# Kernel tuning notes

Measured on AMD Instinct MI355X. Metric: run time of the kernel, lower is better.

The kernel has to match this reference:

```python
import jax, jax.numpy as jnp
import numpy as np

B, S, F_IN, E = 8, 1024, 256, 512
INNER = 2 * E            # mLSTM proj_factor = 2.0
NH = 4                   # mLSTM num_heads
DH = INNER // NH
KS = 4                   # causal conv1d kernel size
QKV_BS = 4               # qkv_proj_blocksize
NB = INNER // QKV_BS     # number of block-diagonal qkv blocks


def setup_inputs() -> dict:
    key = jax.random.key(0)
    ks = jax.random.split(key, 16)
    g = lambda k, shape, scale: jax.random.normal(k, shape, jnp.float32) * scale
    return {
        "x": g(ks[0], (B, S, F_IN), 1.0),
        "W_in": g(ks[1], (E, F_IN), F_IN ** -0.5),
        "b_in": jnp.zeros((E,), jnp.float32),
        "ln1_w": jnp.ones((E,), jnp.float32),
        "W_up": g(ks[2], (2 * INNER, E), E ** -0.5),
        "conv_w": g(ks[3], (INNER, 1, KS), KS ** -0.5),
        "conv_b": jnp.zeros((INNER,), jnp.float32),
        "Wq": g(ks[4], (NB, QKV_BS, QKV_BS), QKV_BS ** -0.5),
        "Wk": g(ks[5], (NB, QKV_BS, QKV_BS), QKV_BS ** -0.5),
        "Wv": g(ks[6], (NB, QKV_BS, QKV_BS), QKV_BS ** -0.5),
        "W_ig": g(ks[7], (NH, 3 * INNER), (3 * INNER) ** -0.5),
        "b_ig": jnp.zeros((NH,), jnp.float32),
        "W_fg": g(ks[8], (NH, 3 * INNER), (3 * INNER) ** -0.5),
        "b_fg": jnp.linspace(3.0, 6.0, NH, dtype=jnp.float32),  # xlstm fgate bias init
        "mhln_w": jnp.ones((INNER,), jnp.float32),
        "skip": jnp.ones((INNER,), jnp.float32),
        "W_down": g(ks[9], (E, INNER), INNER ** -0.5),
        "ln_post_w": jnp.ones((E,), jnp.float32),
    }


def _ln(h, w, eps=1e-5):
    m = h.mean(-1, keepdims=True)
    v = jnp.mean((h - m) ** 2, axis=-1, keepdims=True)
    return (h - m) * jax.lax.rsqrt(v + eps) * w


def _causal_conv(x, w, b):
    # x: (B,S,C) -> depthwise causal conv, kernel KS, left-pad KS-1
    y = jax.lax.conv_general_dilated(
        x.transpose(0, 2, 1), w, (1,), [(KS - 1, 0)],
        dimension_numbers=("NCH", "OIH", "NCH"), feature_group_count=INNER)
    return y.transpose(0, 2, 1) + b


def _headwise(x, W):
    # block-diagonal linear (LinearHeadwiseExpand, bias=False)
    b, s, _ = x.shape
    xh = x.reshape(b, s, NB, QKV_BS)
    return jnp.einsum("bsni,noi->bsno", xh, W).reshape(b, s, -1)


def reference(x, W_in, b_in, ln1_w, W_up, conv_w, conv_b, Wq, Wk, Wv,
              W_ig, b_ig, W_fg, b_fg, mhln_w, skip, W_down, ln_post_w):
    # input proj (+ dropout = identity in eval)
    xp = x @ W_in.T + b_in                                  # (B,S,E)
    res = xp
    h = _ln(xp, ln1_w)                                      # pre-LN of mLSTM block
    up = h @ W_up.T                                         # (B,S,2*INNER)
    x_m, z = up[..., :INNER], up[..., INNER:]
    xc = jax.nn.silu(_causal_conv(x_m, conv_w, conv_b))     # (B,S,INNER)
    q = _headwise(xc, Wq)
    k = _headwise(xc, Wk)
    v = _headwise(x_m, Wv)
    gate_in = jnp.concatenate([q, k, v], axis=-1)           # (B,S,3*INNER)
    ig = (gate_in @ W_ig.T + b_ig).transpose(0, 2, 1)       # (B,NH,S)
    fg = (gate_in @ W_fg.T + b_fg).transpose(0, 2, 1)       # (B,NH,S)
    to_h = lambda t: t.reshape(B, S, NH, DH).transpose(0, 2, 1, 3)
    qh, kh, vh = to_h(q), to_h(k), to_h(v)                  # (B,NH,S,DH)
    # --- parallel_stabilized_simple mLSTM backend ---
    logf = jax.nn.log_sigmoid(fg)                           # (B,NH,S)
    a = jnp.concatenate([jnp.zeros_like(logf[..., :1]), jnp.cumsum(logf, -1)], -1)
    M = a[..., :, None] - a[..., None, :]                   # (B,NH,S+1,S+1)
    mask = jnp.tril(jnp.ones((S + 1, S + 1), bool))
    logD = jnp.where(mask, M, -jnp.inf)[..., 1:, 1:] + ig[..., None, :]
    maxD = logD.max(-1, keepdims=True)                      # (B,NH,S,1)
    D = jnp.exp(logD - maxD)
    C = jnp.einsum("bnsd,bntd->bnst", qh, kh * (DH ** -0.5)) * D
    n = jnp.maximum(jnp.abs(C.sum(-1, keepdims=True)), jnp.exp(-maxD))
    hh = jnp.einsum("bnst,bntd->bnsd", C / (n + 1e-6), vh)  # (B,NH,S,DH)
    # multi-head layernorm (GroupNorm per head, weight only, bias-free)
    hn = hh.transpose(0, 2, 1, 3)                           # (B,S,NH,DH)
    mu = hn.mean(-1, keepdims=True)
    var = jnp.mean((hn - mu) ** 2, axis=-1, keepdims=True)
    hn = (hn - mu) * jax.lax.rsqrt(var + 1e-5) * mhln_w.reshape(NH, DH)
    hn = hn.reshape(B, S, INNER)
    h_state = (hn + skip * xc) * jax.nn.silu(z)             # learnable skip + output gate
    y = h_state @ W_down.T                                  # (B,S,E)
    out = res + y                                           # residual
    return _ln(out, ln_post_w)                              # post_blocks_norm
```

## Files before the change

kernel.cpp:

```cpp
#include <hip/hip_runtime.h>

#define S_LEN 1024
#define B_SZ 8
#define F_IN_D 256
#define E_DIM 512
#define INNER_D 1024
#define NH_D 4
#define DH_D 256
#define NROW (B_SZ * S_LEN)

typedef _Float16 half8 __attribute__((ext_vector_type(8)));
typedef _Float16 half4_t __attribute__((ext_vector_type(4)));
typedef float v4f __attribute__((ext_vector_type(4)));

__global__ __launch_bounds__(256) void cast4_kernel(
    const float* __restrict__ s0, const float* __restrict__ s1,
    const float* __restrict__ s2, const float* __restrict__ s3,
    _Float16* __restrict__ d0, _Float16* __restrict__ d1,
    _Float16* __restrict__ d2, _Float16* __restrict__ d3,
    int n0, int n1, int n2, int n3)
{
  int i = (blockIdx.x * 256 + threadIdx.x) * 4;
  const float* s; _Float16* d; int off;
  if (i < n0)                { s = s0; d = d0; off = i; }
  else if (i < n0 + n1)      { s = s1; d = d1; off = i - n0; }
  else if (i < n0 + n1 + n2) { s = s2; d = d2; off = i - n0 - n1; }
  else if (i < n0 + n1 + n2 + n3) { s = s3; d = d3; off = i - n0 - n1 - n2; }
  else return;
  float4 v = *(const float4*)(s + off);
  half4_t o = {(_Float16)v.x, (_Float16)v.y, (_Float16)v.z, (_Float16)v.w};
  *(half4_t*)(d + off) = o;
}

#define GBM 128
#define GBN 128
#define GBK 64
#define LDKG (GBK + 8)

__global__ __launch_bounds__(256) void gemm_h16(
    const _Float16* __restrict__ A, const _Float16* __restrict__ B,
    const float* __restrict__ bias, float* __restrict__ C,
    int M, int N, int K)
{
  __shared__ __align__(16) _Float16 As[GBM][LDKG];
  __shared__ __align__(16) _Float16 Bs[GBN][LDKG];
  const int tid = threadIdx.x;
  const int lane = tid & 63, w = tid >> 6;
  const int wr = w >> 1, wc = w & 1;
  const int quad = lane >> 4, l16 = lane & 15;
  const int bm = blockIdx.y * GBM, bn = blockIdx.x * GBN;
  const int srow = tid >> 1;
  const int scol = (tid & 1) * 32;

  v4f acc[4][4];
#pragma unroll
  for (int i = 0; i < 4; ++i)
#pragma unroll
    for (int j = 0; j < 4; ++j) acc[i][j] = (v4f){0.f, 0.f, 0.f, 0.f};

  const _Float16* Ap = A + (size_t)(bm + srow) * K + scol;
  const _Float16* Bp = B + (size_t)(bn + srow) * K + scol;
  half8 ap[4], bp[4];
#pragma unroll
  for (int j = 0; j < 4; ++j) {
    ap[j] = *(const half8*)(Ap + j * 8);
    bp[j] = *(const half8*)(Bp + j * 8);
  }

  for (int k0 = 0; k0 < K; k0 += GBK) {
    __syncthreads();
#pragma unroll
    for (int j = 0; j < 4; ++j) {
      *(half8*)(&As[srow][scol + j * 8]) = ap[j];
      *(half8*)(&Bs[srow][scol + j * 8]) = bp[j];
    }
    __syncthreads();
    if (k0 + GBK < K) {
      const int kn = k0 + GBK;
#pragma unroll
      for (int j = 0; j < 4; ++j) {
        ap[j] = *(const half8*)(Ap + kn + j * 8);
        bp[j] = *(const half8*)(Bp + kn + j * 8);
      }
    }
#pragma unroll
    for (int kc = 0; kc < 2; ++kc) {
      half8 af[4], bf[4];
#pragma unroll
      for (int i = 0; i < 4; ++i)
        af[i] = *(const half8*)(&As[wr * 64 + i * 16 + l16][kc * 32 + quad * 8]);
#pragma unroll
      for (int j = 0; j < 4; ++j)
        bf[j] = *(const half8*)(&Bs[wc * 64 + j * 16 + l16][kc * 32 + quad * 8]);
#pragma unroll
      for (int i = 0; i < 4; ++i)
#pragma unroll
        for (int j = 0; j < 4; ++j)
          acc[i][j] = __builtin_amdgcn_mfma_f32_16x16x32_f16(af[i], bf[j], acc[i][j], 0, 0, 0);
    }
  }

#pragma unroll
  for (int j = 0; j < 4; ++j) {
    const int col = bn + wc * 64 + j * 16 + l16;
    const float bv = bias ? bias[col] : 0.f;
#pragma unroll
    for (int i = 0; i < 4; ++i) {
      const int row0 = bm + wr * 64 + i * 16 + quad * 4;
#pragma unroll
      for (int r = 0; r < 4; ++r)
        C[(size_t)(row0 + r) * N + col] = acc[i][j][r] + bv;
    }
  }
}

__global__ __launch_bounds__(256) void gemm_h16_up(
    const _Float16* __restrict__ A, const _Float16* __restrict__ B,
    _Float16* __restrict__ xmh, _Float16* __restrict__ szb,
    int M, int N, int K)
{
  __shared__ __align__(16) _Float16 As[GBM][LDKG];
  __shared__ __align__(16) _Float16 Bs[GBN][LDKG];
  const int tid = threadIdx.x;
  const int lane = tid & 63, w = tid >> 6;
  const int wr = w >> 1, wc = w & 1;
  const int quad = lane >> 4, l16 = lane & 15;
  const int bm = blockIdx.y * GBM, bn = blockIdx.x * GBN;
  const int srow = tid >> 1;
  const int scol = (tid & 1) * 32;

  v4f acc[4][4];
#pragma unroll
  for (int i = 0; i < 4; ++i)
#pragma unroll
    for (int j = 0; j < 4; ++j) acc[i][j] = (v4f){0.f, 0.f, 0.f, 0.f};

  const _Float16* Ap = A + (size_t)(bm + srow) * K + scol;
  const _Float16* Bp = B + (size_t)(bn + srow) * K + scol;
  half8 ap[4], bp[4];
#pragma unroll
  for (int j = 0; j < 4; ++j) {
    ap[j] = *(const half8*)(Ap + j * 8);
    bp[j] = *(const half8*)(Bp + j * 8);
  }

  for (int k0 = 0; k0 < K; k0 += GBK) {
    __syncthreads();
#pragma unroll
    for (int j = 0; j < 4; ++j) {
      *(half8*)(&As[srow][scol + j * 8]) = ap[j];
      *(half8*)(&Bs[srow][scol + j * 8]) = bp[j];
    }
    __syncthreads();
    if (k0 + GBK < K) {
      const int kn = k0 + GBK;
#pragma unroll
      for (int j = 0; j < 4; ++j) {
        ap[j] = *(const half8*)(Ap + kn + j * 8);
        bp[j] = *(const half8*)(Bp + kn + j * 8);
      }
    }
#pragma unroll
    for (int kc = 0; kc < 2; ++kc) {
      half8 af[4], bf[4];
#pragma unroll
      for (int i = 0; i < 4; ++i)
        af[i] = *(const half8*)(&As[wr * 64 + i * 16 + l16][kc * 32 + quad * 8]);
#pragma unroll
      for (int j = 0; j < 4; ++j)
        bf[j] = *(const half8*)(&Bs[wc * 64 + j * 16 + l16][kc * 32 + quad * 8]);
#pragma unroll
      for (int i = 0; i < 4; ++i)
#pragma unroll
        for (int j = 0; j < 4; ++j)
          acc[i][j] = __builtin_amdgcn_mfma_f32_16x16x32_f16(af[i], bf[j], acc[i][j], 0, 0, 0);
    }
  }

  const bool zhalf = (bn >= INNER_D);
#pragma unroll
  for (int j = 0; j < 4; ++j) {
    const int col = bn + wc * 64 + j * 16 + l16;
    const int colm = col & (INNER_D - 1);
#pragma unroll
    for (int i = 0; i < 4; ++i) {
      const int row0 = bm + wr * 64 + i * 16 + quad * 4;
#pragma unroll
      for (int r = 0; r < 4; ++r) {
        float a = acc[i][j][r];
        if (zhalf) {
          float s = a / (1.f + __expf(-a));
          szb[(size_t)(row0 + r) * INNER_D + colm] = (_Float16)s;
        } else {
          xmh[(size_t)(row0 + r) * INNER_D + colm] = (_Float16)a;
        }
      }
    }
  }
}

__device__ __forceinline__ float block_sum4(float v, float* red, int tid) {
#pragma unroll
  for (int off = 32; off; off >>= 1) v += __shfl_xor(v, off);
  if ((tid & 63) == 0) red[tid >> 6] = v;
  __syncthreads();
  float t = red[0] + red[1] + red[2] + red[3];
  __syncthreads();
  return t;
}

__global__ __launch_bounds__(256) void ln_mul_kernel(
    const float* __restrict__ in, const float* __restrict__ w,
    _Float16* __restrict__ out)
{
  __shared__ float red[4];
  const int row = blockIdx.x;
  const int tid = threadIdx.x;
  const float* p = in + (size_t)row * E_DIM;
  float v0 = p[tid], v1 = p[tid + 256];
  float mean = block_sum4(v0 + v1, red, tid) * (1.f / E_DIM);
  float d0 = v0 - mean, d1 = v1 - mean;
  float var = block_sum4(d0 * d0 + d1 * d1, red, tid) * (1.f / E_DIM);
  float rstd = rsqrtf(var + 1e-5f);
  out[(size_t)row * E_DIM + tid] = (_Float16)(d0 * rstd * w[tid]);
  out[(size_t)row * E_DIM + tid + 256] = (_Float16)(d1 * rstd * w[tid + 256]);
}

__global__ __launch_bounds__(256) void final_ln_kernel(
    const float* __restrict__ res, const float* __restrict__ y,
    const float* __restrict__ w, float* __restrict__ out)
{
  __shared__ float red[4];
  const int row = blockIdx.x;
  const int tid = threadIdx.x;
  const size_t base = (size_t)row * E_DIM;
  float v0 = res[base + tid] + y[base + tid];
  float v1 = res[base + tid + 256] + y[base + tid + 256];
  float mean = block_sum4(v0 + v1, red, tid) * (1.f / E_DIM);
  float d0 = v0 - mean, d1 = v1 - mean;
  float var = block_sum4(d0 * d0 + d1 * d1, red, tid) * (1.f / E_DIM);
  float rstd = rsqrtf(var + 1e-5f);
  out[base + tid] = d0 * rstd * w[tid];
  out[base + tid + 256] = d1 * rstd * w[tid + 256];
}

__global__ __launch_bounds__(256) void chg_kernel(
    const _Float16* __restrict__ xm, const float* __restrict__ cw,
    const float* __restrict__ cb,
    const float* __restrict__ Wq, const float* __restrict__ Wk,
    const float* __restrict__ Wv,
    const float* __restrict__ Wig, const float* __restrict__ big,
    const float* __restrict__ Wfg, const float* __restrict__ bfg,
    _Float16* __restrict__ xch, _Float16* __restrict__ qh,
    _Float16* __restrict__ khb, _Float16* __restrict__ vhb,
    float* __restrict__ ig, float* __restrict__ fg)
{
  __shared__ float red[4][32];
  const int tid = threadIdx.x;
  const int lane = tid & 63, wid = tid >> 6;
  const int row0 = blockIdx.x * 4;
  const int sl0 = row0 & (S_LEN - 1);
  const int c = tid * 4;

  float t[7][4];
#pragma unroll
  for (int j = 0; j < 7; ++j) {
    const int off = j - 3;
    if (sl0 + off < 0) {
      t[j][0] = t[j][1] = t[j][2] = t[j][3] = 0.f;
    } else {
      half4_t hv = *(const half4_t*)(xm + (size_t)(row0 + off) * INNER_D + c);
      t[j][0] = (float)hv.x; t[j][1] = (float)hv.y;
      t[j][2] = (float)hv.z; t[j][3] = (float)hv.w;
    }
  }
  float wct[4][4];
#pragma unroll
  for (int j = 0; j < 4; ++j) {
    float4 wc4 = *(const float4*)(cw + (c + j) * 4);
    wct[j][0] = wc4.x; wct[j][1] = wc4.y; wct[j][2] = wc4.z; wct[j][3] = wc4.w;
  }
  float4 cb4 = *(const float4*)(cb + c);
  const float cbs[4] = {cb4.x, cb4.y, cb4.z, cb4.w};
  float wqm[16], wkm[16], wvm[16];
#pragma unroll
  for (int i = 0; i < 4; ++i) {
    float4 a = *(const float4*)(Wq + tid * 16 + i * 4);
    float4 bq = *(const float4*)(Wk + tid * 16 + i * 4);
    float4 cq = *(const float4*)(Wv + tid * 16 + i * 4);
    wqm[i * 4] = a.x; wqm[i * 4 + 1] = a.y; wqm[i * 4 + 2] = a.z; wqm[i * 4 + 3] = a.w;
    wkm[i * 4] = bq.x; wkm[i * 4 + 1] = bq.y; wkm[i * 4 + 2] = bq.z; wkm[i * 4 + 3] = bq.w;
    wvm[i * 4] = cq.x; wvm[i * 4 + 1] = cq.y; wvm[i * 4 + 2] = cq.z; wvm[i * 4 + 3] = cq.w;
  }

  float q4[4][4], k4[4][4], v4m[4][4];
#pragma unroll
  for (int r = 0; r < 4; ++r) {
    float xc4[4];
#pragma unroll
    for (int j = 0; j < 4; ++j) {
      float a = cbs[j] + wct[j][0] * t[r][j] + wct[j][1] * t[r + 1][j]
                       + wct[j][2] * t[r + 2][j] + wct[j][3] * t[r + 3][j];
      xc4[j] = a / (1.f + __expf(-a));
    }
#pragma unroll
    for (int i = 0; i < 4; ++i) {
      q4[r][i] = wqm[i * 4] * xc4[0] + wqm[i * 4 + 1] * xc4[1]
               + wqm[i * 4 + 2] * xc4[2] + wqm[i * 4 + 3] * xc4[3];
      k4[r][i] = wkm[i * 4] * xc4[0] + wkm[i * 4 + 1] * xc4[1]
               + wkm[i * 4 + 2] * xc4[2] + wkm[i * 4 + 3] * xc4[3];
      v4m[r][i] = wvm[i * 4] * t[r + 3][0] + wvm[i * 4 + 1] * t[r + 3][1]
                + wvm[i * 4 + 2] * t[r + 3][2] + wvm[i * 4 + 3] * t[r + 3][3];
    }
    const size_t base = (size_t)(row0 + r) * INNER_D + c;
    half4_t xo = {(_Float16)xc4[0], (_Float16)xc4[1], (_Float16)xc4[2], (_Float16)xc4[3]};
    half4_t qo = {(_Float16)q4[r][0], (_Float16)q4[r][1], (_Float16)q4[r][2], (_Float16)q4[r][3]};
    half4_t ko = {(_Float16)k4[r][0], (_Float16)k4[r][1], (_Float16)k4[r][2], (_Float16)k4[r][3]};
    half4_t vo = {(_Float16)v4m[r][0], (_Float16)v4m[r][1], (_Float16)v4m[r][2], (_Float16)v4m[r][3]};
    *(half4_t*)(xch + base) = xo;
    *(half4_t*)(qh + base) = qo;
    *(half4_t*)(khb + base) = ko;
    *(half4_t*)(vhb + base) = vo;
  }

  float vals[32];
#pragma unroll
  for (int g = 0; g < 8; ++g) {
    const float* wb = (g < 4 ? Wig : Wfg) + (g & 3) * 3072 + c;
    float4 w1 = *(const float4*)(wb);
    float4 w2 = *(const float4*)(wb + 1024);
    float4 w3 = *(const float4*)(wb + 2048);
#pragma unroll
    for (int r = 0; r < 4; ++r) {
      vals[g * 4 + r] =
          q4[r][0] * w1.x + q4[r][1] * w1.y + q4[r][2] * w1.z + q4[r][3] * w1.w
        + k4[r][0] * w2.x + k4[r][1] * w2.y + k4[r][2] * w2.z + k4[r][3] * w2.w
        + v4m[r][0] * w3.x + v4m[r][1] * w3.y + v4m[r][2] * w3.z + v4m[r][3] * w3.w;
    }
  }
#pragma unroll
  for (int i = 0; i < 32; ++i) {
    float x = vals[i];
#pragma unroll
    for (int off = 32; off; off >>= 1) x += __shfl_xor(x, off);
    vals[i] = x;
  }
  if (lane == 0) {
#pragma unroll
    for (int i = 0; i < 32; ++i) red[wid][i] = vals[i];
  }
  __syncthreads();
  if (tid < 32) {
    float sm = red[0][tid] + red[1][tid] + red[2][tid] + red[3][tid];
    const int g = tid >> 2, r = tid & 3;
    const int h = g & 3;
    const int b = row0 >> 10;
    const size_t oidx = (size_t)(b * NH_D + h) * S_LEN + sl0 + r;
    if (g < 4) ig[oidx] = sm + big[h];
    else       fg[oidx] = sm + bfg[h];
  }
}

__device__ __forceinline__ float logsigf(float x) {
  return fminf(x, 0.f) - log1pf(__expf(-fabsf(x)));
}

__global__ __launch_bounds__(256) void scan_kernel(
    const float* __restrict__ ig, const float* __restrict__ fg,
    float* __restrict__ m_, float* __restrict__ rmax_, float* __restrict__ maxd_,
    float* __restrict__ em_)
{
  __shared__ float sc[256];
  const int bh = blockIdx.x;
  const int tid = threadIdx.x;
  const size_t base = (size_t)bh * S_LEN + tid * 4;
  float4 f4 = *(const float4*)(fg + base);
  float4 i4 = *(const float4*)(ig + base);
  float l0 = logsigf(f4.x), l1 = logsigf(f4.y), l2 = logsigf(f4.z), l3 = logsigf(f4.w);
  float p0 = l0, p1 = p0 + l1, p2 = p1 + l2, p3 = p2 + l3;
  sc[tid] = p3;
  __syncthreads();
  for (int off = 1; off < 256; off <<= 1) {
    float o = (tid >= off) ? sc[tid - off] : 0.f;
    __syncthreads();
    sc[tid] += o;
    __syncthreads();
  }
  float aoff = (tid == 0) ? 0.f : sc[tid - 1];
  __syncthreads();
  float a0 = aoff + p0, a1 = aoff + p1, a2 = aoff + p2, a3 = aoff + p3;
  float m0 = i4.x - a0, m1 = i4.y - a1, m2 = i4.z - a2, m3 = i4.w - a3;
  float x0 = m0, x1 = fmaxf(x0, m1), x2 = fmaxf(x1, m2), x3 = fmaxf(x2, m3);
  sc[tid] = x3;
  __syncthreads();
  for (int off = 1; off < 256; off <<= 1) {
    float o = (tid >= off) ? sc[tid - off] : -1e30f;
    __syncthreads();
    sc[tid] = fmaxf(sc[tid], o);
    __syncthreads();
  }
  float moff = (tid == 0) ? -1e30f : sc[tid - 1];
  float tmax = sc[tid | 15];
  float r0 = fmaxf(moff, x0), r1 = fmaxf(moff, x1), r2 = fmaxf(moff, x2), r3 = fmaxf(moff, x3);
  const float scale = 0.0625f;
  float4 mo = {m0, m1, m2, m3};
  float4 ro = {r0, r1, r2, r3};
  float4 dd = {a0 + r0, a1 + r1, a2 + r2, a3 + r3};
  float4 eo = {scale * __expf(m0 - tmax), scale * __expf(m1 - tmax),
               scale * __expf(m2 - tmax), scale * __expf(m3 - tmax)};
  *(float4*)(m_ + base) = mo;
  *(float4*)(rmax_ + base) = ro;
  *(float4*)(maxd_ + base) = dd;
  *(float4*)(em_ + base) = eo;
}

__global__ __launch_bounds__(256) void vtrans_kernel(
    const _Float16* __restrict__ vb, _Float16* __restrict__ vt)
{
  __shared__ _Float16 tile[64][68];
  const int b = blockIdx.z, dt = blockIdx.x, st = blockIdx.y;
  const int c4 = (threadIdx.x & 15) * 4, rr = threadIdx.x >> 4;
  const int s0 = st * 64, d0 = dt * 64;
#pragma unroll
  for (int i = 0; i < 4; ++i) {
    int r = rr + i * 16;
    half4_t v = *(const half4_t*)(vb + ((size_t)(b * S_LEN + s0 + r)) * INNER_D + d0 + c4);
    tile[r][c4 + 0] = v.x; tile[r][c4 + 1] = v.y;
    tile[r][c4 + 2] = v.z; tile[r][c4 + 3] = v.w;
  }
  __syncthreads();
#pragma unroll
  for (int i = 0; i < 4; ++i) {
    int dd = rr + i * 16;
    half4_t o = {tile[c4 + 0][dd], tile[c4 + 1][dd], tile[c4 + 2][dd], tile[c4 + 3][dd]};
    *(half4_t*)(vt + ((size_t)(b * INNER_D + d0 + dd)) * S_LEN + s0 + c4) = o;
  }
}

#define KP 264
#define VP 72

__global__ __launch_bounds__(256, 2) void attn_blk_kernel(
    const _Float16* __restrict__ qh, const _Float16* __restrict__ khb,
    const _Float16* __restrict__ vt,
    const float* __restrict__ m_, const float* __restrict__ em,
    const float* __restrict__ rmax_, const float* __restrict__ maxd_,
    const float* __restrict__ mhln_w, const float* __restrict__ skip,
    const _Float16* __restrict__ xch, const _Float16* __restrict__ szb,
    _Float16* __restrict__ hstate)
{
  __shared__ __align__(16) _Float16 Ks[64][KP];
  __shared__ __align__(16) _Float16 Vs[256][VP];
  __shared__ _Float16 plds[4][16][72];
  const int tid = threadIdx.x;
  const int lane = tid & 63, wid = tid >> 6;
  const int quad = lane >> 4, l16 = lane & 15;
  const int bh = blockIdx.x & 31;
  const int pp = blockIdx.x >> 5;
  const int sblk = 15 - pp;
  const int h = bh & 3, b = bh >> 2;
  _Float16 (*P)[72] = plds[wid];
  const float* rmaxp = rmax_ + (size_t)bh * S_LEN;
  const float* emp = em + (size_t)bh * S_LEN;
  const float* mp = m_ + (size_t)bh * S_LEN;
  const float* maxdp = maxd_ + (size_t)bh * S_LEN;
  const float scale = 0.0625f;

  const _Float16* kg = khb + ((size_t)(b * S_LEN)) * INNER_D + h * DH_D;
  const _Float16* vg = vt + ((size_t)(b * INNER_D + h * DH_D)) * S_LEN;
  const int krow_s = tid >> 5;
  const int kcol_s = (tid & 31) * 8;
  const int vrow_s = tid >> 3;
  const int vcol_s = (tid & 7) * 8;

  const int ntile = sblk + 1;
  const int s0 = sblk * 64 + wid * 16;

  half8 kpre[8], vpre[8];
#pragma unroll
  for (int i = 0; i < 8; ++i) {
    kpre[i] = *(const half8*)(kg + (size_t)(i * 8 + krow_s) * INNER_D + kcol_s);
    vpre[i] = *(const half8*)(vg + (size_t)(i * 32 + vrow_s) * S_LEN + vcol_s);
  }

  half8 qf[8];
  const _Float16* qrow = qh + ((size_t)(b * S_LEN + s0 + l16)) * INNER_D + h * DH_D + quad * 8;
#pragma unroll
  for (int c = 0; c < 8; ++c) qf[c] = *(const half8*)(qrow + c * 32);

  v4f acc[16];
#pragma unroll
  for (int nc = 0; nc < 16; ++nc) acc[nc] = (v4f){0.f, 0.f, 0.f, 0.f};
  float rsum[4] = {0.f, 0.f, 0.f, 0.f};
  float rmax_row[4];
#pragma unroll
  for (int r = 0; r < 4; ++r) rmax_row[r] = rmaxp[s0 + quad * 4 + r];

  for (int tt = 0; tt < ntile; ++tt) {
    const int t0 = tt * 64;
    const bool last = (tt + 1 == ntile);
    __syncthreads();
#pragma unroll
    for (int i = 0; i < 8; ++i) {
      *(half8*)(&Ks[i * 8 + krow_s][kcol_s]) = kpre[i];
      *(half8*)(&Vs[i * 32 + vrow_s][vcol_s]) = vpre[i];
    }
    __syncthreads();
    if (!last) {
      const int tn = t0 + 64;
#pragma unroll
      for (int i = 0; i < 8; ++i) {
        kpre[i] = *(const half8*)(kg + (size_t)(tn + i * 8 + krow_s) * INNER_D + kcol_s);
        vpre[i] = *(const half8*)(vg + (size_t)(i * 32 + vrow_s) * S_LEN + tn + vcol_s);
      }
    }
    const bool diag = last;
    float rowfac[4];
    if (!diag) {
      const float rtile = rmaxp[t0 + 63];
#pragma unroll
      for (int r = 0; r < 4; ++r) rowfac[r] = __expf(rtile - rmax_row[r]);
    }
#pragma unroll
    for (int sub = 0; sub < 4; ++sub) {
      v4f sacc0 = (v4f){0.f, 0.f, 0.f, 0.f};
      v4f sacc1 = (v4f){0.f, 0.f, 0.f, 0.f};
#pragma unroll
      for (int c = 0; c < 4; ++c) {
        half8 kf0 = *(const half8*)(&Ks[sub * 16 + l16][c * 32 + quad * 8]);
        half8 kf1 = *(const half8*)(&Ks[sub * 16 + l16][(c + 4) * 32 + quad * 8]);
        sacc0 = __builtin_amdgcn_mfma_f32_16x16x32_f16(qf[c], kf0, sacc0, 0, 0, 0);
        sacc1 = __builtin_amdgcn_mfma_f32_16x16x32_f16(qf[c + 4], kf1, sacc1, 0, 0, 0);
      }
      v4f sacc = sacc0 + sacc1;
      const int t = t0 + sub * 16 + l16;
      if (diag) {
        const float mt = mp[t];
#pragma unroll
        for (int r = 0; r < 4; ++r) {
          const int srow = s0 + quad * 4 + r;
          float cc = (t <= srow) ? sacc[r] * scale * __expf(mt - rmax_row[r]) : 0.f;
          rsum[r] += cc;
          P[quad * 4 + r][sub * 16 + l16] = (_Float16)cc;
        }
      } else {
        const float emv = emp[t];
#pragma unroll
        for (int r = 0; r < 4; ++r) {
          float cc = sacc[r] * emv * rowfac[r];
          rsum[r] += cc;
          P[quad * 4 + r][sub * 16 + l16] = (_Float16)cc;
        }
      }
    }
    asm volatile("s_waitcnt lgkmcnt(0)" ::: "memory");
    half8 pf0 = *(const half8*)(&P[l16][quad * 8]);
    half8 pf1 = *(const half8*)(&P[l16][32 + quad * 8]);
#pragma unroll
    for (int nc = 0; nc < 16; ++nc) {
      half8 vf0 = *(const half8*)(&Vs[nc * 16 + l16][quad * 8]);
      half8 vf1 = *(const half8*)(&Vs[nc * 16 + l16][32 + quad * 8]);
      acc[nc] = __builtin_amdgcn_mfma_f32_16x16x32_f16(pf0, vf0, acc[nc], 0, 0, 0);
      acc[nc] = __builtin_amdgcn_mfma_f32_16x16x32_f16(pf1, vf1, acc[nc], 0, 0, 0);
    }
  }

  float inv[4];
#pragma unroll
  for (int r = 0; r < 4; ++r) {
    float rs = rsum[r];
    rs += __shfl_xor(rs, 1); rs += __shfl_xor(rs, 2);
    rs += __shfl_xor(rs, 4); rs += __shfl_xor(rs, 8);
    float md = maxdp[s0 + quad * 4 + r];
    float n = fmaxf(fabsf(rs), __expf(-md));
    inv[r] = 1.f / (n + 1e-6f);
  }
#pragma unroll
  for (int nc = 0; nc < 16; ++nc) {
#pragma unroll
    for (int r = 0; r < 4; ++r) acc[nc][r] *= inv[r];
  }
  float mean[4], rstd[4];
#pragma unroll
  for (int r = 0; r < 4; ++r) {
    float sm = 0.f;
#pragma unroll
    for (int nc = 0; nc < 16; ++nc) sm += acc[nc][r];
    sm += __shfl_xor(sm, 1); sm += __shfl_xor(sm, 2);
    sm += __shfl_xor(sm, 4); sm += __shfl_xor(sm, 8);
    mean[r] = sm * (1.f / DH_D);
  }
#pragma unroll
  for (int r = 0; r < 4; ++r) {
    float sq = 0.f;
#pragma unroll
    for (int nc = 0; nc < 16; ++nc) { float d = acc[nc][r] - mean[r]; sq += d * d; }
    sq += __shfl_xor(sq, 1); sq += __shfl_xor(sq, 2);
    sq += __shfl_xor(sq, 4); sq += __shfl_xor(sq, 8);
    rstd[r] = rsqrtf(sq * (1.f / DH_D) + 1e-5f);
  }
#pragma unroll
  for (int nc = 0; nc < 16; ++nc) {
    const int d = h * DH_D + nc * 16 + l16;
    const float w = mhln_w[d];
    const float sk = skip[d];
#pragma unroll
    for (int r = 0; r < 4; ++r) {
      const size_t row = (size_t)(b * S_LEN + s0 + quad * 4 + r);
      float xcv = (float)xch[row * INNER_D + d];
      float sz = (float)szb[row * INNER_D + d];
      float o = ((acc[nc][r] - mean[r]) * rstd[r] * w + sk * xcv) * sz;
      hstate[row * INNER_D + d] = (_Float16)o;
    }
  }
}

extern "C" void kernel_launch(void* const* d_in, const int* in_sizes, int n_in,
                              void* d_out, int out_size, void* d_ws, size_t ws_size,
                              hipStream_t stream)
{
  const float* x      = (const float*)d_in[0];
  const float* W_in   = (const float*)d_in[1];
  const float* b_in   = (const float*)d_in[2];
  const float* ln1_w  = (const float*)d_in[3];
  const float* W_up   = (const float*)d_in[4];
  const float* conv_w = (const float*)d_in[5];
  const float* conv_b = (const float*)d_in[6];
  const float* Wq     = (const float*)d_in[7];
  const float* Wk     = (const float*)d_in[8];
  const float* Wv     = (const float*)d_in[9];
  const float* W_ig   = (const float*)d_in[10];
  const float* b_ig   = (const float*)d_in[11];
  const float* W_fg   = (const float*)d_in[12];
  const float* b_fg   = (const float*)d_in[13];
  const float* mhln_w = (const float*)d_in[14];
  const float* skip   = (const float*)d_in[15];
  const float* W_down = (const float*)d_in[16];
  const float* ln_post_w = (const float*)d_in[17];
  float* out = (float*)d_out;

  float* ws = (float*)d_ws;
  size_t o = 0;
  float* xp     = ws + o; o += (size_t)NROW * E_DIM;
  float* hbuf   = ws + o; o += (size_t)NROW * E_DIM;
  _Float16* h16 = (_Float16*)(ws + o);
  size_t ho = 0;
  _Float16* xh      = h16 + ho; ho += (size_t)NROW * F_IN_D;
  _Float16* WinH    = h16 + ho; ho += (size_t)E_DIM * F_IN_D;
  _Float16* WupH    = h16 + ho; ho += (size_t)2 * INNER_D * E_DIM;
  _Float16* WdownH  = h16 + ho; ho += (size_t)E_DIM * INNER_D;
  _Float16* hh      = h16 + ho; ho += (size_t)NROW * E_DIM;
  _Float16* xmh     = h16 + ho; ho += (size_t)NROW * INNER_D;
  _Float16* szb     = h16 + ho; ho += (size_t)NROW * INNER_D;
  _Float16* xch     = h16 + ho; ho += (size_t)NROW * INNER_D;
  _Float16* qh      = h16 + ho; ho += (size_t)NROW * INNER_D;
  _Float16* khb     = h16 + ho; ho += (size_t)NROW * INNER_D;
  _Float16* vhb     = h16 + ho; ho += (size_t)NROW * INNER_D;
  _Float16* vtb     = h16 + ho; ho += (size_t)NROW * INNER_D;
  _Float16* hstateH = h16 + ho; ho += (size_t)NROW * INNER_D;

  const int GSZ = B_SZ * NH_D * S_LEN;
  float* igb   = hbuf;
  float* fgb   = hbuf + GSZ;
  float* mb    = hbuf + 2 * GSZ;
  float* rmaxb = hbuf + 3 * GSZ;
  float* maxdb = hbuf + 4 * GSZ;
  float* emb   = hbuf + 5 * GSZ;
  float* yb    = hbuf;

  dim3 blk(256);
  const int nx = NROW * F_IN_D, nwi = E_DIM * F_IN_D,
            nwu = 2 * INNER_D * E_DIM, nwd = E_DIM * INNER_D;
  const int ntot = nx + nwi + nwu + nwd;
  cast4_kernel<<<(ntot / 4 + 255) / 256, blk, 0, stream>>>(
      x, W_in, W_up, W_down, xh, WinH, WupH, WdownH, nx, nwi, nwu, nwd);
  gemm_h16<<<dim3(E_DIM / GBN, NROW / GBM), blk, 0, stream>>>(
      xh, WinH, b_in, xp, NROW, E_DIM, F_IN_D);
  ln_mul_kernel<<<NROW, blk, 0, stream>>>(xp, ln1_w, hh);
  gemm_h16_up<<<dim3(2 * INNER_D / GBN, NROW / GBM), blk, 0, stream>>>(
      hh, WupH, xmh, szb, NROW, 2 * INNER_D, E_DIM);
  chg_kernel<<<NROW / 4, blk, 0, stream>>>(
      xmh, conv_w, conv_b, Wq, Wk, Wv, W_ig, b_ig, W_fg, b_fg,
      xch, qh, khb, vhb, igb, fgb);
  scan_kernel<<<B_SZ * NH_D, blk, 0, stream>>>(igb, fgb, mb, rmaxb, maxdb, emb);
  vtrans_kernel<<<dim3(16, 16, 8), blk, 0, stream>>>(vhb, vtb);
  attn_blk_kernel<<<512, blk, 0, stream>>>(
      qh, khb, vtb, mb, emb, rmaxb, maxdb, mhln_w, skip, xch, szb, hstateH);
  gemm_h16<<<dim3(E_DIM / GBN, NROW / GBM), blk, 0, stream>>>(
      hstateH, WdownH, nullptr, yb, NROW, E_DIM, INNER_D);
  final_ln_kernel<<<NROW, blk, 0, stream>>>(xp, yb, ln_post_w, out);
}
```

Measured before the change: 281.6 us.

## Retile mLSTM attention waves into 2x2 grid sharing K/V fragments

```diff
diff --git a/kernel.cpp b/kernel.cpp
--- a/kernel.cpp
+++ b/kernel.cpp
@@ -439,6 +439,7 @@
 
 #define KP 264
 #define VP 72
+#define PP 72
 
 __global__ __launch_bounds__(256, 2) void attn_blk_kernel(
     const _Float16* __restrict__ qh, const _Float16* __restrict__ khb,
@@ -451,15 +452,18 @@
 {
   __shared__ __align__(16) _Float16 Ks[64][KP];
   __shared__ __align__(16) _Float16 Vs[256][VP];
-  __shared__ _Float16 plds[4][16][72];
+  __shared__ __align__(16) _Float16 Pl[64][PP];
+  __shared__ float cred[2][64];
   const int tid = threadIdx.x;
   const int lane = tid & 63, wid = tid >> 6;
   const int quad = lane >> 4, l16 = lane & 15;
+  const int wr = wid >> 1;
+  const int ws = wid & 1;
   const int bh = blockIdx.x & 31;
-  const int pp = blockIdx.x >> 5;
+  int pp = blockIdx.x >> 5;
+  if (pp >= 8) pp = 23 - pp;
   const int sblk = 15 - pp;
   const int h = bh & 3, b = bh >> 2;
-  _Float16 (*P)[72] = plds[wid];
   const float* rmaxp = rmax_ + (size_t)bh * S_LEN;
   const float* emp = em + (size_t)bh * S_LEN;
   const float* mp = m_ + (size_t)bh * S_LEN;
@@ -474,7 +478,7 @@
   const int vcol_s = (tid & 7) * 8;
 
   const int ntile = sblk + 1;
-  const int s0 = sblk * 64 + wid * 16;
+  const int qb0 = sblk * 64;
 
   half8 kpre[8], vpre[8];
 #pragma unroll
@@ -483,18 +487,28 @@
     vpre[i] = *(const half8*)(vg + (size_t)(i * 32 + vrow_s) * S_LEN + vcol_s);
   }
 
-  half8 qf[8];
-  const _Float16* qrow = qh + ((size_t)(b * S_LEN + s0 + l16)) * INNER_D + h * DH_D + quad * 8;
-#pragma unroll
-  for (int c = 0; c < 8; ++c) qf[c] = *(const half8*)(qrow + c * 32);
-
-  v4f acc[16];
-#pragma unroll
-  for (int nc = 0; nc < 16; ++nc) acc[nc] = (v4f){0.f, 0.f, 0.f, 0.f};
-  float rsum[4] = {0.f, 0.f, 0.f, 0.f};
-  float rmax_row[4];
-#pragma unroll
-  for (int r = 0; r < 4; ++r) rmax_row[r] = rmaxp[s0 + quad * 4 + r];
+  half8 qf[2][8];
+#pragma unroll
+  for (int g = 0; g < 2; ++g) {
+    const _Float16* qrow =
+        qh + ((size_t)(b * S_LEN + qb0 + wr * 32 + g * 16 + l16)) * INNER_D
+           + h * DH_D + quad * 8;
+#pragma unroll
+    for (int c = 0; c < 8; ++c) qf[g][c] = *(const half8*)(qrow + c * 32);
+  }
+
+  v4f acc[2][8];
+#pragma unroll
+  for (int g = 0; g < 2; ++g)
+#pragma unroll
+    for (int nc = 0; nc < 8; ++nc) acc[g][nc] = (v4f){0.f, 0.f, 0.f, 0.f};
+  float rsum[8] = {0.f, 0.f, 0.f, 0.f, 0.f, 0.f, 0.f, 0.f};
+  float rmax_row[8];
+#pragma unroll
+  for (int g = 0; g < 2; ++g)
+#pragma unroll
+    for (int r = 0; r < 4; ++r)
+      rmax_row[g * 4 + r] = rmaxp[qb0 + wr * 32 + g * 16 + quad * 4 + r];
 
   for (int tt = 0; tt < ntile; ++tt) {
     const int t0 = tt * 64;
@@ -514,104 +528,153 @@
         vpre[i] = *(const half8*)(vg + (size_t)(i * 32 + vrow_s) * S_LEN + tn + vcol_s);
       }
     }
-    const bool diag = last;
-    float rowfac[4];
-    if (!diag) {
+    float rowfac[8];
+    if (!last) {
       const float rtile = rmaxp[t0 + 63];
 #pragma unroll
-      for (int r = 0; r < 4; ++r) rowfac[r] = __expf(rtile - rmax_row[r]);
-    }
-#pragma unroll
-    for (int sub = 0; sub < 4; ++sub) {
-      v4f sacc0 = (v4f){0.f, 0.f, 0.f, 0.f};
-      v4f sacc1 = (v4f){0.f, 0.f, 0.f, 0.f};
-#pragma unroll
-      for (int c = 0; c < 4; ++c) {
-        half8 kf0 = *(const half8*)(&Ks[sub * 16 + l16][c * 32 + quad * 8]);
-        half8 kf1 = *(const half8*)(&Ks[sub * 16 + l16][(c + 4) * 32 + quad * 8]);
-        sacc0 = __builtin_amdgcn_mfma_f32_16x16x32_f16(qf[c], kf0, sacc0, 0, 0, 0);
-        sacc1 = __builtin_amdgcn_mfma_f32_16x16x32_f16(qf[c + 4], kf1, sacc1, 0, 0, 0);
+      for (int gr = 0; gr < 8; ++gr) rowfac[gr] = __expf(rtile - rmax_row[gr]);
+    }
+#pragma unroll
+    for (int ks = 0; ks < 2; ++ks) {
+      v4f sg[2];
+      sg[0] = (v4f){0.f, 0.f, 0.f, 0.f};
+      sg[1] = (v4f){0.f, 0.f, 0.f, 0.f};
+#pragma unroll
+      for (int c = 0; c < 8; ++c) {
+        half8 kf = *(const half8*)(&Ks[ws * 32 + ks * 16 + l16][c * 32 + quad * 8]);
+        sg[0] = __builtin_amdgcn_mfma_f32_16x16x32_f16(qf[0][c], kf, sg[0], 0, 0, 0);
+        sg[1] = __builtin_amdgcn_mfma_f32_16x16x32_f16(qf[1][c], kf, sg[1], 0, 0, 0);
       }
-      v4f sacc = sacc0 + sacc1;
-      const int t = t0 + sub * 16 + l16;
-      if (diag) {
+      const int t = t0 + ws * 32 + ks * 16 + l16;
+      if (last) {
         const float mt = mp[t];
 #pragma unroll
-        for (int r = 0; r < 4; ++r) {
-          const int srow = s0 + quad * 4 + r;
-          float cc = (t <= srow) ? sacc[r] * scale * __expf(mt - rmax_row[r]) : 0.f;
-          rsum[r] += cc;
-          P[quad * 4 + r][sub * 16 + l16] = (_Float16)cc;
-        }
+        for (int g = 0; g < 2; ++g)
+#pragma unroll
+          for (int r = 0; r < 4; ++r) {
+            const int srow = qb0 + wr * 32 + g * 16 + quad * 4 + r;
+            float cc = (t <= srow)
+                         ? sg[g][r] * scale * __expf(mt - rmax_row[g * 4 + r]) : 0.f;
+            rsum[g * 4 + r] += cc;
+            Pl[wr * 32 + g * 16 + quad * 4 + r][ws * 32 + ks * 16 + l16] = (_Float16)cc;
+          }
       } else {
         const float emv = emp[t];
 #pragma unroll
-        for (int r = 0; r < 4; ++r) {
-          float cc = sacc[r] * emv * rowfac[r];
-          rsum[r] += cc;
-          P[quad * 4 + r][sub * 16 + l16] = (_Float16)cc;
-        }
+        for (int g = 0; g < 2; ++g)
+#pragma unroll
+          for (int r = 0; r < 4; ++r) {
+            float cc = sg[g][r] * emv * rowfac[g * 4 + r];
+            rsum[g * 4 + r] += cc;
+            Pl[wr * 32 + g * 16 + quad * 4 + r][ws * 32 + ks * 16 + l16] = (_Float16)cc;
+          }
       }
     }
-    asm volatile("s_waitcnt lgkmcnt(0)" ::: "memory");
-    half8 pf0 = *(const half8*)(&P[l16][quad * 8]);
-    half8 pf1 = *(const half8*)(&P[l16][32 + quad * 8]);
-#pragma unroll
-    for (int nc = 0; nc < 16; ++nc) {
-      half8 vf0 = *(const half8*)(&Vs[nc * 16 + l16][quad * 8]);
-      half8 vf1 = *(const half8*)(&Vs[nc * 16 + l16][32 + quad * 8]);
-      acc[nc] = __builtin_amdgcn_mfma_f32_16x16x32_f16(pf0, vf0, acc[nc], 0, 0, 0);
-      acc[nc] = __builtin_amdgcn_mfma_f32_16x16x32_f16(pf1, vf1, acc[nc], 0, 0, 0);
-    }
-  }
-
-  float inv[4];
-#pragma unroll
-  for (int r = 0; r < 4; ++r) {
-    float rs = rsum[r];
+    __syncthreads();
+    half8 pf[2][2];
+#pragma unroll
+    for (int g = 0; g < 2; ++g) {
+      pf[g][0] = *(const half8*)(&Pl[wr * 32 + g * 16 + l16][quad * 8]);
+      pf[g][1] = *(const half8*)(&Pl[wr * 32 + g * 16 + l16][32 + quad * 8]);
+    }
+#pragma unroll
+    for (int nc = 0; nc < 8; ++nc) {
+      half8 vf0 = *(const half8*)(&Vs[ws * 128 + nc * 16 + l16][quad * 8]);
+      half8 vf1 = *(const half8*)(&Vs[ws * 128 + nc * 16 + l16][32 + quad * 8]);
+      acc[0][nc] = __builtin_amdgcn_mfma_f32_16x16x32_f16(pf[0][0], vf0, acc[0][nc], 0, 0, 0);
+      acc[0][nc] = __builtin_amdgcn_mfma_f32_16x16x32_f16(pf[0][1], vf1, acc[0][nc], 0, 0, 0);
+      acc[1][nc] = __builtin_amdgcn_mfma_f32_16x16x32_f16(pf[1][0], vf0, acc[1][nc], 0, 0, 0);
+      acc[1][nc] = __builtin_amdgcn_mfma_f32_16x16x32_f16(pf[1][1], vf1, acc[1][nc], 0, 0, 0);
+    }
+  }
+
+#pragma unroll
+  for (int gr = 0; gr < 8; ++gr) {
+    float rs = rsum[gr];
     rs += __shfl_xor(rs, 1); rs += __shfl_xor(rs, 2);
     rs += __shfl_xor(rs, 4); rs += __shfl_xor(rs, 8);
-    float md = maxdp[s0 + quad * 4 + r];
-    float n = fmaxf(fabsf(rs), __expf(-md));
-    inv[r] = 1.f / (n + 1e-6f);
-  }
-#pragma unroll
-  for (int nc = 0; nc < 16; ++nc) {
-#pragma unroll
-    for (int r = 0; r < 4; ++r) acc[nc][r] *= inv[r];
-  }
-  float mean[4], rstd[4];
-#pragma unroll
-  for (int r = 0; r < 4; ++r) {
+    rsum[gr] = rs;
+  }
+  if (l16 == 0) {
+#pragma unroll
+    for (int g = 0; g < 2; ++g)
+#pragma unroll
+      for (int r = 0; r < 4; ++r)
+        cred[ws][wr * 32 + g * 16 + quad * 4 + r] = rsum[g * 4 + r];
+  }
+  __syncthreads();
+  float inv[8];
+#pragma unroll
+  for (int g = 0; g < 2; ++g)
+#pragma unroll
+    for (int r = 0; r < 4; ++r) {
+      const int row = wr * 32 + g * 16 + quad * 4 + r;
+      float rs = cred[0][row] + cred[1][row];
+      float md = maxdp[qb0 + row];
+      float n = fmaxf(fabsf(rs), __expf(-md));
+      inv[g * 4 + r] = 1.f / (n + 1e-6f);
+    }
+#pragma unroll
+  for (int g = 0; g < 2; ++g)
+#pragma unroll
+    for (int nc = 0; nc < 8; ++nc)
+#pragma unroll
+      for (int r = 0; r < 4; ++r) acc[g][nc][r] *= inv[g * 4 + r];
+
+  __syncthreads();
+  float mean[8];
+#pragma unroll
+  for (int gr = 0; gr < 8; ++gr) {
+    const int g = gr >> 2, r = gr & 3;
     float sm = 0.f;
 #pragma unroll
-    for (int nc = 0; nc < 16; ++nc) sm += acc[nc][r];
+    for (int nc = 0; nc < 8; ++nc) sm += acc[g][nc][r];
     sm += __shfl_xor(sm, 1); sm += __shfl_xor(sm, 2);
     sm += __shfl_xor(sm, 4); sm += __shfl_xor(sm, 8);
-    mean[r] = sm * (1.f / DH_D);
-  }
-#pragma unroll
-  for (int r = 0; r < 4; ++r) {
+    if (l16 == 0) cred[ws][wr * 32 + g * 16 + quad * 4 + r] = sm;
+  }
+  __syncthreads();
+#pragma unroll
+  for (int gr = 0; gr < 8; ++gr) {
+    const int g = gr >> 2, r = gr & 3;
+    const int row = wr * 32 + g * 16 + quad * 4 + r;
+    mean[gr] = (cred[0][row] + cred[1][row]) * (1.f / DH_D);
+  }
+  __syncthreads();
+  float rstd[8];
+#pragma unroll
+  for (int gr = 0; gr < 8; ++gr) {
+    const int g = gr >> 2, r = gr & 3;
     float sq = 0.f;
 #pragma unroll
-    for (int nc = 0; nc < 16; ++nc) { float d = acc[nc][r] - mean[r]; sq += d * d; }
+    for (int nc = 0; nc < 8; ++nc) { float d = acc[g][nc][r] - mean[gr]; sq += d * d; }
     sq += __shfl_xor(sq, 1); sq += __shfl_xor(sq, 2);
     sq += __shfl_xor(sq, 4); sq += __shfl_xor(sq, 8);
-    rstd[r] = rsqrtf(sq * (1.f / DH_D) + 1e-5f);
-  }
-#pragma unroll
-  for (int nc = 0; nc < 16; ++nc) {
-    const int d = h * DH_D + nc * 16 + l16;
+    if (l16 == 0) cred[ws][wr * 32 + g * 16 + quad * 4 + r] = sq;
+  }
+  __syncthreads();
+#pragma unroll
+  for (int gr = 0; gr < 8; ++gr) {
+    const int g = gr >> 2, r = gr & 3;
+    const int row = wr * 32 + g * 16 + quad * 4 + r;
+    rstd[gr] = rsqrtf((cred[0][row] + cred[1][row]) * (1.f / DH_D) + 1e-5f);
+  }
+
+#pragma unroll
+  for (int nc = 0; nc < 8; ++nc) {
+    const int d = h * DH_D + ws * 128 + nc * 16 + l16;
     const float w = mhln_w[d];
     const float sk = skip[d];
 #pragma unroll
-    for (int r = 0; r < 4; ++r) {
-      const size_t row = (size_t)(b * S_LEN + s0 + quad * 4 + r);
-      float xcv = (float)xch[row * INNER_D + d];
-      float sz = (float)szb[row * INNER_D + d];
-      float o = ((acc[nc][r] - mean[r]) * rstd[r] * w + sk * xcv) * sz;
-      hstate[row * INNER_D + d] = (_Float16)o;
-    }
+    for (int g = 0; g < 2; ++g)
+#pragma unroll
+      for (int r = 0; r < 4; ++r) {
+        const size_t row = (size_t)(b * S_LEN + qb0 + wr * 32 + g * 16 + quad * 4 + r);
+        float xcv = (float)xch[row * INNER_D + d];
+        float sz = (float)szb[row * INNER_D + d];
+        float o = ((acc[g][nc][r] - mean[g * 4 + r]) * rstd[g * 4 + r] * w + sk * xcv) * sz;
+        hstate[row * INNER_D + d] = (_Float16)o;
+      }
   }
 }
 
```

Result: no change. 283.9 us (+0.8%).

## Use direct global-to-LDS loads with double-buffered swizzled tiles in fp16 GEMMs

Applied to the files above, without the earlier changes.

```diff
diff --git a/kernel.cpp b/kernel.cpp
--- a/kernel.cpp
+++ b/kernel.cpp
@@ -32,25 +32,35 @@
   *(half4_t*)(d + off) = o;
 }
 
+__device__ __forceinline__ void gl_lds16(const _Float16* g, _Float16* l) {
+  __builtin_amdgcn_global_load_lds(
+      (const __attribute__((address_space(1))) void*)g,
+      (__attribute__((address_space(3))) void*)l, 16, 0, 0);
+}
+
 #define GBM 128
 #define GBN 128
 #define GBK 64
-#define LDKG (GBK + 8)
 
 __global__ __launch_bounds__(256) void gemm_h16(
     const _Float16* __restrict__ A, const _Float16* __restrict__ B,
     const float* __restrict__ bias, float* __restrict__ C,
     int M, int N, int K)
 {
-  __shared__ __align__(16) _Float16 As[GBM][LDKG];
-  __shared__ __align__(16) _Float16 Bs[GBN][LDKG];
+  __shared__ __align__(16) _Float16 As[2][GBM][GBK];
+  __shared__ __align__(16) _Float16 Bs[2][GBN][GBK];
   const int tid = threadIdx.x;
   const int lane = tid & 63, w = tid >> 6;
   const int wr = w >> 1, wc = w & 1;
   const int quad = lane >> 4, l16 = lane & 15;
   const int bm = blockIdx.y * GBM, bn = blockIdx.x * GBN;
-  const int srow = tid >> 1;
-  const int scol = (tid & 1) * 32;
+
+  const int srow = lane >> 3;
+  const int scolh = ((lane & 7) * 8) ^ (srow << 3);
+  const _Float16* Ag = A + (size_t)(bm + w * 32 + srow) * K + scolh;
+  const _Float16* Bg = B + (size_t)(bn + w * 32 + srow) * K + scolh;
+
+  const int rswz = (l16 & 7) << 3;
 
   v4f acc[4][4];
 #pragma unroll
@@ -58,29 +68,21 @@
 #pragma unroll
     for (int j = 0; j < 4; ++j) acc[i][j] = (v4f){0.f, 0.f, 0.f, 0.f};
 
-  const _Float16* Ap = A + (size_t)(bm + srow) * K + scol;
-  const _Float16* Bp = B + (size_t)(bn + srow) * K + scol;
-  half8 ap[4], bp[4];
-#pragma unroll
-  for (int j = 0; j < 4; ++j) {
-    ap[j] = *(const half8*)(Ap + j * 8);
-    bp[j] = *(const half8*)(Bp + j * 8);
-  }
-
+#pragma unroll
+  for (int i = 0; i < 4; ++i) {
+    gl_lds16(Ag + (size_t)(i * 8) * K, &As[0][w * 32 + i * 8][0]);
+    gl_lds16(Bg + (size_t)(i * 8) * K, &Bs[0][w * 32 + i * 8][0]);
+  }
+  __syncthreads();
+
+  int buf = 0;
   for (int k0 = 0; k0 < K; k0 += GBK) {
-    __syncthreads();
-#pragma unroll
-    for (int j = 0; j < 4; ++j) {
-      *(half8*)(&As[srow][scol + j * 8]) = ap[j];
-      *(half8*)(&Bs[srow][scol + j * 8]) = bp[j];
-    }
-    __syncthreads();
     if (k0 + GBK < K) {
       const int kn = k0 + GBK;
 #pragma unroll
-      for (int j = 0; j < 4; ++j) {
-        ap[j] = *(const half8*)(Ap + kn + j * 8);
-        bp[j] = *(const half8*)(Bp + kn + j * 8);
+      for (int i = 0; i < 4; ++i) {
+        gl_lds16(Ag + (size_t)(i * 8) * K + kn, &As[buf ^ 1][w * 32 + i * 8][0]);
+        gl_lds16(Bg + (size_t)(i * 8) * K + kn, &Bs[buf ^ 1][w * 32 + i * 8][0]);
       }
     }
 #pragma unroll
@@ -88,16 +90,18 @@
       half8 af[4], bf[4];
 #pragma unroll
       for (int i = 0; i < 4; ++i)
-        af[i] = *(const half8*)(&As[wr * 64 + i * 16 + l16][kc * 32 + quad * 8]);
+        af[i] = *(const half8*)(&As[buf][wr * 64 + i * 16 + l16][(kc * 32 + quad * 8) ^ rswz]);
 #pragma unroll
       for (int j = 0; j < 4; ++j)
-        bf[j] = *(const half8*)(&Bs[wc * 64 + j * 16 + l16][kc * 32 + quad * 8]);
+        bf[j] = *(const half8*)(&Bs[buf][wc * 64 + j * 16 + l16][(kc * 32 + quad * 8) ^ rswz]);
 #pragma unroll
       for (int i = 0; i < 4; ++i)
 #pragma unroll
         for (int j = 0; j < 4; ++j)
           acc[i][j] = __builtin_amdgcn_mfma_f32_16x16x32_f16(af[i], bf[j], acc[i][j], 0, 0, 0);
     }
+    __syncthreads();
+    buf ^= 1;
   }
 
 #pragma unroll
@@ -119,15 +123,19 @@
     _Float16* __restrict__ xmh, _Float16* __restrict__ szb,
     int M, int N, int K)
 {
-  __shared__ __align__(16) _Float16 As[GBM][LDKG];
-  __shared__ __align__(16) _Float16 Bs[GBN][LDKG];
+  __shared__ __align__(16) _Float16 As[2][GBM][GBK];
+  __shared__ __align__(16) _Float16 Bs[2][GBN][GBK];
   const int tid = threadIdx.x;
   const int lane = tid & 63, w = tid >> 6;
   const int wr = w >> 1, wc = w & 1;
   const int quad = lane >> 4, l16 = lane & 15;
   const int bm = blockIdx.y * GBM, bn = blockIdx.x * GBN;
-  const int srow = tid >> 1;
-  const int scol = (tid & 1) * 32;
+
+  const int srow = lane >> 3;
+  const int scolh = ((lane & 7) * 8) ^ (srow << 3);
+  const _Float16* Ag = A + (size_t)(bm + w * 32 + srow) * K + scolh;
+  const _Float16* Bg = B + (size_t)(bn + w * 32 + srow) * K + scolh;
+  const int rswz = (l16 & 7) << 3;
 
   v4f acc[4][4];
 #pragma unroll
@@ -135,29 +143,21 @@
 #pragma unroll
     for (int j = 0; j < 4; ++j) acc[i][j] = (v4f){0.f, 0.f, 0.f, 0.f};
 
-  const _Float16* Ap = A + (size_t)(bm + srow) * K + scol;
-  const _Float16* Bp = B + (size_t)(bn + srow) * K + scol;
-  half8 ap[4], bp[4];
-#pragma unroll
-  for (int j = 0; j < 4; ++j) {
-    ap[j] = *(const half8*)(Ap + j * 8);
-    bp[j] = *(const half8*)(Bp + j * 8);
-  }
-
+#pragma unroll
+  for (int i = 0; i < 4; ++i) {
+    gl_lds16(Ag + (size_t)(i * 8) * K, &As[0][w * 32 + i * 8][0]);
+    gl_lds16(Bg + (size_t)(i * 8) * K, &Bs[0][w * 32 + i * 8][0]);
+  }
+  __syncthreads();
+
+  int buf = 0;
   for (int k0 = 0; k0 < K; k0 += GBK) {
-    __syncthreads();
-#pragma unroll
-    for (int j = 0; j < 4; ++j) {
-      *(half8*)(&As[srow][scol + j * 8]) = ap[j];
-      *(half8*)(&Bs[srow][scol + j * 8]) = bp[j];
-    }
-    __syncthreads();
     if (k0 + GBK < K) {
       const int kn = k0 + GBK;
 #pragma unroll
-      for (int j = 0; j < 4; ++j) {
-        ap[j] = *(const half8*)(Ap + kn + j * 8);
-        bp[j] = *(const half8*)(Bp + kn + j * 8);
+      for (int i = 0; i < 4; ++i) {
+        gl_lds16(Ag + (size_t)(i * 8) * K + kn, &As[buf ^ 1][w * 32 + i * 8][0]);
+        gl_lds16(Bg + (size_t)(i * 8) * K + kn, &Bs[buf ^ 1][w * 32 + i * 8][0]);
       }
     }
 #pragma unroll
@@ -165,16 +165,18 @@
       half8 af[4], bf[4];
 #pragma unroll
       for (int i = 0; i < 4; ++i)
-        af[i] = *(const half8*)(&As[wr * 64 + i * 16 + l16][kc * 32 + quad * 8]);
+        af[i] = *(const half8*)(&As[buf][wr * 64 + i * 16 + l16][(kc * 32 + quad * 8) ^ rswz]);
 #pragma unroll
       for (int j = 0; j < 4; ++j)
-        bf[j] = *(const half8*)(&Bs[wc * 64 + j * 16 + l16][kc * 32 + quad * 8]);
+        bf[j] = *(const half8*)(&Bs[buf][wc * 64 + j * 16 + l16][(kc * 32 + quad * 8) ^ rswz]);
 #pragma unroll
       for (int i = 0; i < 4; ++i)
 #pragma unroll
         for (int j = 0; j < 4; ++j)
           acc[i][j] = __builtin_amdgcn_mfma_f32_16x16x32_f16(af[i], bf[j], acc[i][j], 0, 0, 0);
     }
+    __syncthreads();
+    buf ^= 1;
   }
 
   const bool zhalf = (bn >= INNER_D);
```

Result: slower. 295.1 us (+4.8%).
